# Performance work log

Measured on AMD Instinct MI355X. Metric: run time of the kernel, lower is better.

The kernel has to match this reference:

```python
import jax, jax.numpy as jnp
import numpy as np
import math

B, S, D = 2, 2048, 1024
H, DK, DV = 16, 64, 64  # head_count, query_size, value_size; H*DV == D
NEG_INF = -jnp.inf


def setup_inputs() -> dict:
    key = jax.random.key(0)
    ks = jax.random.split(key, 10)
    sc = 0.02
    return {
        "input": jax.random.normal(ks[0], (B, S, D), dtype=jnp.float32),
        "padding_mask": jnp.zeros((B, S), dtype=jnp.float32),  # 0 = valid, 1 = padded
        "wq_w": jax.random.normal(ks[1], (H * DK, D), dtype=jnp.float32) * sc,
        "wq_b": jnp.zeros((H * DK,), dtype=jnp.float32),
        "wk_w": jax.random.normal(ks[2], (H * DK, D), dtype=jnp.float32) * sc,
        "wk_b": jnp.zeros((H * DK,), dtype=jnp.float32),
        "wv_w": jax.random.normal(ks[3], (H * DV, D), dtype=jnp.float32) * sc,
        "wv_b": jnp.zeros((H * DV,), dtype=jnp.float32),
        "fin_w": jax.random.normal(ks[4], (D, H * DV), dtype=jnp.float32) * sc,
        "fin_b": jnp.zeros((D,), dtype=jnp.float32),
    }


def reference(input, padding_mask, wq_w, wq_b, wk_w, wk_b, wv_w, wv_b, fin_w, fin_b):
    b, s, _ = input.shape
    # projections -> [b, h, s, d]
    Q = (input @ wq_w.T + wq_b).reshape(b, s, H, DK).transpose(0, 2, 1, 3)
    K = (input @ wk_w.T + wk_b).reshape(b, s, H, DK).transpose(0, 2, 1, 3)
    V = (input @ wv_w.T + wv_b).reshape(b, s, H, DV).transpose(0, 2, 1, 3)

    # padding mask: pad*(-inf), nan_to_num(0*inf -> 0); broadcast over query dim
    pad = jnp.where(padding_mask > 0, NEG_INF, 0.0)[:, None, None, :]  # [b,1,1,s]
    i = jnp.arange(s)
    causal = jnp.where(i[None, :] < i[:, None] + 1, 0.0, NEG_INF)  # [s,s]
    mask = pad + causal[None, None, :, :]

    # (QK^T + mask) / sqrt(dk), softmax over keys
    logits = (jnp.einsum("bhqd,bhkd->bhqk", Q, K) + mask) / math.sqrt(DK)
    attn = jax.nn.softmax(logits, axis=-1)
    out = jnp.einsum("bhqk,bhkd->bqhd", attn, V).reshape(b, s, H * DV)
    return out @ fin_w.T + fin_b
```

## Files before the change

kernel.cpp:

```cpp
#include <hip/hip_runtime.h>


typedef __bf16 bf16;
typedef __bf16 bf16x8 __attribute__((ext_vector_type(8)));
typedef __bf16 bf16x4 __attribute__((ext_vector_type(4)));
typedef float  f32x4  __attribute__((ext_vector_type(4)));

#define B_  2
#define S_  2048
#define D_  1024
#define H_  16
#define HD  64
#define NEG_BIG (-3.0e38f)
#define SCALE_LOG2E 0.1803368801111204f

__device__ __forceinline__ void lds16(const void* g, void* l) {
    __builtin_amdgcn_global_load_lds((const __attribute__((address_space(1))) void*)g,
                                     (__attribute__((address_space(3))) void*)l, 16, 0, 0);
}

__device__ __forceinline__ f32x4 mfma16(bf16x8 a, bf16x8 b, f32x4 c) {
    return __builtin_amdgcn_mfma_f32_16x16x32_bf16(a, b, c, 0, 0, 0);
}

__global__ __launch_bounds__(256) void convert_k(const float* __restrict__ X,
                                                 const float* __restrict__ wq,
                                                 const float* __restrict__ wk,
                                                 const float* __restrict__ wv,
                                                 const float* __restrict__ wo,
                                                 bf16* __restrict__ dst) {
    const int gid = blockIdx.x * 256 + threadIdx.x;
    const int i   = gid * 4;
    const float* src;
    int off;
    if      (i < (4 << 20)) { src = X;  off = 0; }
    else if (i < (5 << 20)) { src = wq; off = 4 << 20; }
    else if (i < (6 << 20)) { src = wk; off = 5 << 20; }
    else if (i < (7 << 20)) { src = wv; off = 6 << 20; }
    else                    { src = wo; off = 7 << 20; }
    const float4 v = *(const float4*)(src + (i - off));
    bf16x4 p;
    p[0] = (bf16)v.x; p[1] = (bf16)v.y; p[2] = (bf16)v.z; p[3] = (bf16)v.w;
    *(bf16x4*)(dst + i) = p;
}

__global__ __launch_bounds__(256) void gemm_qkv(const bf16* __restrict__ A,
                                                const bf16* __restrict__ Wq,
                                                const bf16* __restrict__ Wk,
                                                const bf16* __restrict__ Wv,
                                                const float* __restrict__ bq,
                                                const float* __restrict__ bk,
                                                const float* __restrict__ bv,
                                                bf16* __restrict__ Qw,
                                                bf16* __restrict__ Kw,
                                                bf16* __restrict__ Vw) {
    constexpr int K = 1024;
    __shared__ bf16 sA[128 * 32];
    __shared__ bf16 sB[128 * 32];
    const int tid  = threadIdx.x;
    const int l15  = tid & 15;
    const int quad = (tid & 63) >> 4;
    const int wid  = tid >> 6;
    const int seg  = blockIdx.x >> 3;
    const int bn   = blockIdx.x & 7;
    const int bm   = blockIdx.y;
    const int wm   = (wid >> 1) * 64;
    const int wn   = (wid & 1) * 64;

    const bf16* W    = (seg == 0) ? Wq : (seg == 1) ? Wk : Wv;
    const float* bias = (seg == 0) ? bq : (seg == 1) ? bk : bv;

    const bf16* Ab = A + (size_t)bm * 128 * K;
    const bf16* Wb = W + (size_t)bn * 128 * K;

    f32x4 acc[4][4] = {};

    for (int k0 = 0; k0 < K; k0 += 32) {
        __syncthreads();
        #pragma unroll
        for (int it = 0; it < 2; ++it) {
            int c = it * 256 + tid;
            int row = c >> 2, c8 = c & 3;
            lds16(Ab + row * K + k0 + c8 * 8, (char*)sA + c * 16);
            lds16(Wb + row * K + k0 + c8 * 8, (char*)sB + c * 16);
        }
        __syncthreads();
        bf16x8 af[4], bfr[4];
        #pragma unroll
        for (int i = 0; i < 4; ++i)
            af[i] = *(const bf16x8*)&sA[(wm + i * 16 + l15) * 32 + quad * 8];
        #pragma unroll
        for (int i = 0; i < 4; ++i)
            bfr[i] = *(const bf16x8*)&sB[(wn + i * 16 + l15) * 32 + quad * 8];
        #pragma unroll
        for (int mi = 0; mi < 4; ++mi)
            #pragma unroll
            for (int ni = 0; ni < 4; ++ni)
                acc[mi][ni] = mfma16(af[mi], bfr[ni], acc[mi][ni]);
    }

    #pragma unroll
    for (int ni = 0; ni < 4; ++ni) {
        const int n  = bn * 128 + wn + ni * 16 + l15;
        const float bv_ = bias[n];
        const int h = n >> 6;
        #pragma unroll
        for (int mi = 0; mi < 4; ++mi) {
            const int m0 = bm * 128 + wm + mi * 16 + quad * 4;
            if (seg == 2) {
                const int dv = n & 63;
                const int b = m0 >> 11, s = m0 & 2047;
                bf16x4 pack;
                #pragma unroll
                for (int r = 0; r < 4; ++r) pack[r] = (bf16)(acc[mi][ni][r] + bv_);
                *(bf16x4*)&Vw[(((size_t)(b * H_ + h) * HD + dv) << 11) + s] = pack;
            } else {
                bf16* C = (seg == 0) ? Qw : Kw;
                const int dk = n & 63;
                #pragma unroll
                for (int r = 0; r < 4; ++r) {
                    const int m = m0 + r, b = m >> 11, s = m & 2047;
                    C[(((size_t)(b * H_ + h) << 11) + s) * HD + dk] =
                        (bf16)(acc[mi][ni][r] + bv_);
                }
            }
        }
    }
}

__global__ __launch_bounds__(256) void gemm_fin(const bf16* __restrict__ A,
                                                const bf16* __restrict__ W,
                                                const float* __restrict__ bias,
                                                float* __restrict__ C) {
    constexpr int N = 1024, K = 1024;
    __shared__ bf16 sA[128 * 32];
    __shared__ bf16 sB[128 * 32];
    const int tid  = threadIdx.x;
    const int l15  = tid & 15;
    const int quad = (tid & 63) >> 4;
    const int wid  = tid >> 6;
    const int bm   = blockIdx.x >> 3;
    const int bn   = blockIdx.x & 7;
    const int wm   = (wid >> 1) * 64;
    const int wn   = (wid & 1) * 64;

    const bf16* Ab = A + (size_t)bm * 128 * K;
    const bf16* Wb = W + (size_t)bn * 128 * K;

    f32x4 acc[4][4] = {};

    for (int k0 = 0; k0 < K; k0 += 32) {
        __syncthreads();
        #pragma unroll
        for (int it = 0; it < 2; ++it) {
            int c = it * 256 + tid;
            int row = c >> 2, c8 = c & 3;
            lds16(Ab + row * K + k0 + c8 * 8, (char*)sA + c * 16);
            lds16(Wb + row * K + k0 + c8 * 8, (char*)sB + c * 16);
        }
        __syncthreads();
        bf16x8 af[4], bfr[4];
        #pragma unroll
        for (int i = 0; i < 4; ++i)
            af[i] = *(const bf16x8*)&sA[(wm + i * 16 + l15) * 32 + quad * 8];
        #pragma unroll
        for (int i = 0; i < 4; ++i)
            bfr[i] = *(const bf16x8*)&sB[(wn + i * 16 + l15) * 32 + quad * 8];
        #pragma unroll
        for (int mi = 0; mi < 4; ++mi)
            #pragma unroll
            for (int ni = 0; ni < 4; ++ni)
                acc[mi][ni] = mfma16(af[mi], bfr[ni], acc[mi][ni]);
    }

    #pragma unroll
    for (int ni = 0; ni < 4; ++ni) {
        const int n  = bn * 128 + wn + ni * 16 + l15;
        const float bv = bias[n];
        #pragma unroll
        for (int mi = 0; mi < 4; ++mi) {
            const int m0 = bm * 128 + wm + mi * 16 + quad * 4;
            #pragma unroll
            for (int r = 0; r < 4; ++r)
                C[(size_t)(m0 + r) * N + n] = acc[mi][ni][r] + bv;
        }
    }
}

__global__ __launch_bounds__(512, 4) void attn_k(const bf16* __restrict__ Q,
                                                 const bf16* __restrict__ K,
                                                 const bf16* __restrict__ Vt,
                                                 const float* __restrict__ pmask,
                                                 bf16* __restrict__ Aout) {
    __shared__ bf16 sK_[2 * 128 * 32];
    __shared__ bf16 sV[4 * 64 * 32];
    __shared__ bf16 sPQ[4 * 128 * 32];
    const int tid  = threadIdx.x;
    const int l15  = tid & 15;
    const int quad = (tid & 63) >> 4;
    const int wid  = tid >> 6;
    const int idx  = blockIdx.x >> 5;
    const int qt   = (idx < 8) ? (15 - idx) : (idx - 8);
    const int bh   = blockIdx.x & 31;
    const int b    = bh >> 4;
    const int h    = bh & 15;

    const bf16* Qg = Q + ((size_t)bh * S_ + qt * 128) * HD;
    #pragma unroll
    for (int it = 0; it < 2; ++it) {
        int c = it * 512 + tid;
        int pl = c >> 9, row = (c >> 2) & 127, c8 = c & 3;
        lds16(Qg + row * HD + pl * 32 + c8 * 8, (char*)sPQ + c * 16);
    }
    __syncthreads();
    bf16x8 aq[2];
    #pragma unroll
    for (int kk = 0; kk < 2; ++kk)
        aq[kk] = *(const bf16x8*)&sPQ[(kk * 128 + wid * 16 + l15) * 32 + quad * 8];

    float m_i[4], l_i[4];
    f32x4 o[4] = {};
    #pragma unroll
    for (int r = 0; r < 4; ++r) { m_i[r] = NEG_BIG; l_i[r] = 0.f; }

    for (int kt = 0; kt <= qt; ++kt) {
        __syncthreads();
        const bf16* Kg = K  + ((size_t)bh * S_ + kt * 128) * HD;
        const bf16* Vg = Vt + (size_t)bh * HD * S_ + kt * 128;
        #pragma unroll
        for (int it = 0; it < 2; ++it) {
            int c = it * 512 + tid;
            { int pl = c >> 9, row = (c >> 2) & 127, c8 = c & 3;
              lds16(Kg + row * HD + pl * 32 + c8 * 8, (char*)sK_ + c * 16); }
            { int kc = c >> 8, dv = (c >> 2) & 63, c8 = c & 3;
              lds16(Vg + dv * S_ + kc * 32 + c8 * 8, (char*)sV + c * 16); }
        }
        __syncthreads();

        f32x4 s[8] = {};
        #pragma unroll
        for (int tc = 0; tc < 8; ++tc) {
            #pragma unroll
            for (int kk = 0; kk < 2; ++kk) {
                bf16x8 bk = *(const bf16x8*)
                    &sK_[(kk * 128 + tc * 16 + l15) * 32 + quad * 8];
                s[tc] = mfma16(aq[kk], bk, s[tc]);
            }
        }

        float pmadd[8];
        #pragma unroll
        for (int tc = 0; tc < 8; ++tc) {
            int kg = kt * 128 + tc * 16 + l15;
            pmadd[tc] = (pmask[b * S_ + kg] > 0.f) ? NEG_BIG : 0.f;
        }
        const bool diag = (kt == qt);
        #pragma unroll
        for (int tc = 0; tc < 8; ++tc)
            #pragma unroll
            for (int r = 0; r < 4; ++r) {
                float v = s[tc][r] * SCALE_LOG2E + pmadd[tc];
                if (diag) {
                    int kl = tc * 16 + l15;
                    int ql = wid * 16 + quad * 4 + r;
                    if (kl > ql) v = NEG_BIG;
                }
                s[tc][r] = v;
            }

        #pragma unroll
        for (int r = 0; r < 4; ++r) {
            float rm = s[0][r];
            #pragma unroll
            for (int tc = 1; tc < 8; ++tc) rm = fmaxf(rm, s[tc][r]);
            rm = fmaxf(rm, __shfl_xor(rm, 1, 16));
            rm = fmaxf(rm, __shfl_xor(rm, 2, 16));
            rm = fmaxf(rm, __shfl_xor(rm, 4, 16));
            rm = fmaxf(rm, __shfl_xor(rm, 8, 16));
            float mn    = fmaxf(m_i[r], rm);
            float alpha = exp2f(m_i[r] - mn);
            m_i[r]      = mn;
            float rs = 0.f;
            #pragma unroll
            for (int tc = 0; tc < 8; ++tc) {
                float p = exp2f(s[tc][r] - mn);
                s[tc][r] = p;
                rs += p;
            }
            rs += __shfl_xor(rs, 1, 16);
            rs += __shfl_xor(rs, 2, 16);
            rs += __shfl_xor(rs, 4, 16);
            rs += __shfl_xor(rs, 8, 16);
            l_i[r] = l_i[r] * alpha + rs;
            #pragma unroll
            for (int vc = 0; vc < 4; ++vc) o[vc][r] *= alpha;
        }

        #pragma unroll
        for (int tc = 0; tc < 8; ++tc)
            #pragma unroll
            for (int r = 0; r < 4; ++r) {
                int ql = wid * 16 + quad * 4 + r;
                int kl = tc * 16 + l15;
                sPQ[((kl >> 5) * 128 + ql) * 32 + (kl & 31)] = (bf16)s[tc][r];
            }
        __syncthreads();

        #pragma unroll
        for (int kc = 0; kc < 4; ++kc) {
            bf16x8 ap = *(const bf16x8*)
                &sPQ[(kc * 128 + wid * 16 + l15) * 32 + quad * 8];
            #pragma unroll
            for (int vc = 0; vc < 4; ++vc) {
                bf16x8 bv = *(const bf16x8*)
                    &sV[(kc * 64 + vc * 16 + l15) * 32 + quad * 8];
                o[vc] = mfma16(ap, bv, o[vc]);
            }
        }
    }

    #pragma unroll
    for (int r = 0; r < 4; ++r) {
        float inv = 1.f / l_i[r];
        int q = qt * 128 + wid * 16 + quad * 4 + r;
        size_t base = ((size_t)b * S_ + q) * D_ + h * HD;
        #pragma unroll
        for (int vc = 0; vc < 4; ++vc)
            Aout[base + vc * 16 + l15] = (bf16)(o[vc][r] * inv);
    }
}

extern "C" void kernel_launch(void* const* d_in, const int* in_sizes, int n_in,
                              void* d_out, int out_size, void* d_ws, size_t ws_size,
                              hipStream_t stream) {
    const float* X   = (const float*)d_in[0];
    const float* pm  = (const float*)d_in[1];
    const float* wq  = (const float*)d_in[2];
    const float* bq  = (const float*)d_in[3];
    const float* wk  = (const float*)d_in[4];
    const float* bk  = (const float*)d_in[5];
    const float* wv  = (const float*)d_in[6];
    const float* bvb = (const float*)d_in[7];
    const float* wo  = (const float*)d_in[8];
    const float* bo  = (const float*)d_in[9];
    float* out = (float*)d_out;

    char* ws = (char*)d_ws;
    bf16* Xb  = (bf16*)(ws);
    bf16* Wqb = (bf16*)(ws + (8u  << 20));
    bf16* Wkb = (bf16*)(ws + (10u << 20));
    bf16* Wvb = (bf16*)(ws + (12u << 20));
    bf16* Wob = (bf16*)(ws + (14u << 20));
    bf16* Qw  = (bf16*)(ws + (16u << 20));
    bf16* Kw  = (bf16*)(ws + (24u << 20));
    bf16* Vw  = (bf16*)(ws + (32u << 20));
    bf16* Aw  = (bf16*)(ws + (40u << 20));

    convert_k<<<dim3(8192), dim3(256), 0, stream>>>(X, wq, wk, wv, wo, Xb);
    gemm_qkv<<<dim3(24, 32), dim3(256), 0, stream>>>(Xb, Wqb, Wkb, Wvb,
                                                     bq, bk, bvb, Qw, Kw, Vw);
    attn_k<<<dim3(512), dim3(512), 0, stream>>>(Qw, Kw, Vw, pm, Aw);
    gemm_fin<<<dim3(256), dim3(256), 0, stream>>>(Aw, Wob, bo, out);
}
```

Before: 221.8 us.

## Prefetch next K/V tile into registers and transpose S for row-local softmax

The attention kernel now loads the next K/V tile from global memory into registers while the current tile is being computed, then stores those registers into LDS at the start of the next iteration, replacing the synchronous LDS-direct loads. The QK^T MFMA operands are swapped so each lane holds one query row's scores. This lets the row max and row sum use two cross-quad shuffles instead of four per row, and lets P be written as packed bf16x4 into a padded row-major LDS buffer. The padding mask is read as a float4. The cost is more registers for the prefetch buffers and extra shuffles to broadcast alpha and 1/l into the output layout, which may reduce occupancy.

```diff
diff --git a/kernel.cpp b/kernel.cpp
--- a/kernel.cpp
+++ b/kernel.cpp
@@ -187,6 +187,7 @@
     }
 }
 
+#define PSTRIDE 136
 __global__ __launch_bounds__(512, 4) void attn_k(const bf16* __restrict__ Q,
                                                  const bf16* __restrict__ K,
                                                  const bf16* __restrict__ Vt,
@@ -194,7 +195,7 @@
                                                  bf16* __restrict__ Aout) {
     __shared__ bf16 sK_[2 * 128 * 32];
     __shared__ bf16 sV[4 * 64 * 32];
-    __shared__ bf16 sPQ[4 * 128 * 32];
+    __shared__ bf16 sP[128 * PSTRIDE];
     const int tid  = threadIdx.x;
     const int l15  = tid & 15;
     const int quad = (tid & 63) >> 4;
@@ -210,30 +211,50 @@
     for (int it = 0; it < 2; ++it) {
         int c = it * 512 + tid;
         int pl = c >> 9, row = (c >> 2) & 127, c8 = c & 3;
-        lds16(Qg + row * HD + pl * 32 + c8 * 8, (char*)sPQ + c * 16);
+        lds16(Qg + row * HD + pl * 32 + c8 * 8, (char*)sP + c * 16);
+    }
+    bf16x8 kreg[2], vreg[2];
+    {
+        const bf16* Kg = K  + (size_t)bh * S_ * HD;
+        const bf16* Vg = Vt + (size_t)bh * HD * S_;
+        #pragma unroll
+        for (int it = 0; it < 2; ++it) {
+            int c = it * 512 + tid;
+            int pl = c >> 9, row = (c >> 2) & 127, c8 = c & 3;
+            kreg[it] = *(const bf16x8*)(Kg + row * HD + pl * 32 + c8 * 8);
+            int kc = c >> 8, dv = (c >> 2) & 63;
+            vreg[it] = *(const bf16x8*)(Vg + dv * S_ + kc * 32 + c8 * 8);
+        }
     }
     __syncthreads();
     bf16x8 aq[2];
     #pragma unroll
     for (int kk = 0; kk < 2; ++kk)
-        aq[kk] = *(const bf16x8*)&sPQ[(kk * 128 + wid * 16 + l15) * 32 + quad * 8];
-
-    float m_i[4], l_i[4];
+        aq[kk] = *(const bf16x8*)&sP[(kk * 128 + wid * 16 + l15) * 32 + quad * 8];
+
+    float m_i = NEG_BIG, l_i = 0.f;
     f32x4 o[4] = {};
-    #pragma unroll
-    for (int r = 0; r < 4; ++r) { m_i[r] = NEG_BIG; l_i[r] = 0.f; }
+    const int qg = wid * 16 + l15;
 
     for (int kt = 0; kt <= qt; ++kt) {
         __syncthreads();
-        const bf16* Kg = K  + ((size_t)bh * S_ + kt * 128) * HD;
-        const bf16* Vg = Vt + (size_t)bh * HD * S_ + kt * 128;
         #pragma unroll
         for (int it = 0; it < 2; ++it) {
             int c = it * 512 + tid;
-            { int pl = c >> 9, row = (c >> 2) & 127, c8 = c & 3;
-              lds16(Kg + row * HD + pl * 32 + c8 * 8, (char*)sK_ + c * 16); }
-            { int kc = c >> 8, dv = (c >> 2) & 63, c8 = c & 3;
-              lds16(Vg + dv * S_ + kc * 32 + c8 * 8, (char*)sV + c * 16); }
+            *(bf16x8*)((char*)sK_ + c * 16) = kreg[it];
+            *(bf16x8*)((char*)sV  + c * 16) = vreg[it];
+        }
+        if (kt < qt) {
+            const bf16* Kg = K  + ((size_t)bh * S_ + (kt + 1) * 128) * HD;
+            const bf16* Vg = Vt + (size_t)bh * HD * S_ + (kt + 1) * 128;
+            #pragma unroll
+            for (int it = 0; it < 2; ++it) {
+                int c = it * 512 + tid;
+                int pl = c >> 9, row = (c >> 2) & 127, c8 = c & 3;
+                kreg[it] = *(const bf16x8*)(Kg + row * HD + pl * 32 + c8 * 8);
+                int kc = c >> 8, dv = (c >> 2) & 63;
+                vreg[it] = *(const bf16x8*)(Vg + dv * S_ + kc * 32 + c8 * 8);
+            }
         }
         __syncthreads();
 
@@ -242,74 +263,69 @@
         for (int tc = 0; tc < 8; ++tc) {
             #pragma unroll
             for (int kk = 0; kk < 2; ++kk) {
-                bf16x8 bk = *(const bf16x8*)
+                bf16x8 kb = *(const bf16x8*)
                     &sK_[(kk * 128 + tc * 16 + l15) * 32 + quad * 8];
-                s[tc] = mfma16(aq[kk], bk, s[tc]);
-            }
-        }
-
-        float pmadd[8];
+                s[tc] = mfma16(kb, aq[kk], s[tc]);
+            }
+        }
+
+        const bool diag = (kt == qt);
         #pragma unroll
         for (int tc = 0; tc < 8; ++tc) {
-            int kg = kt * 128 + tc * 16 + l15;
-            pmadd[tc] = (pmask[b * S_ + kg] > 0.f) ? NEG_BIG : 0.f;
-        }
-        const bool diag = (kt == qt);
+            const float4 pv = *(const float4*)
+                &pmask[b * S_ + kt * 128 + tc * 16 + quad * 4];
+            #pragma unroll
+            for (int r = 0; r < 4; ++r) {
+                float v = s[tc][r] * SCALE_LOG2E;
+                if (((const float*)&pv)[r] > 0.f) v = NEG_BIG;
+                if (diag && (tc * 16 + quad * 4 + r > qg)) v = NEG_BIG;
+                s[tc][r] = v;
+            }
+        }
+
+        float rm = s[0][0];
         #pragma unroll
         for (int tc = 0; tc < 8; ++tc)
             #pragma unroll
+            for (int r = 0; r < 4; ++r) rm = fmaxf(rm, s[tc][r]);
+        rm = fmaxf(rm, __shfl_xor(rm, 16));
+        rm = fmaxf(rm, __shfl_xor(rm, 32));
+        const float mn    = fmaxf(m_i, rm);
+        const float alpha = exp2f(m_i - mn);
+        m_i = mn;
+        float rs = 0.f;
+        #pragma unroll
+        for (int tc = 0; tc < 8; ++tc)
+            #pragma unroll
             for (int r = 0; r < 4; ++r) {
-                float v = s[tc][r] * SCALE_LOG2E + pmadd[tc];
-                if (diag) {
-                    int kl = tc * 16 + l15;
-                    int ql = wid * 16 + quad * 4 + r;
-                    if (kl > ql) v = NEG_BIG;
-                }
-                s[tc][r] = v;
-            }
-
-        #pragma unroll
-        for (int r = 0; r < 4; ++r) {
-            float rm = s[0][r];
-            #pragma unroll
-            for (int tc = 1; tc < 8; ++tc) rm = fmaxf(rm, s[tc][r]);
-            rm = fmaxf(rm, __shfl_xor(rm, 1, 16));
-            rm = fmaxf(rm, __shfl_xor(rm, 2, 16));
-            rm = fmaxf(rm, __shfl_xor(rm, 4, 16));
-            rm = fmaxf(rm, __shfl_xor(rm, 8, 16));
-            float mn    = fmaxf(m_i[r], rm);
-            float alpha = exp2f(m_i[r] - mn);
-            m_i[r]      = mn;
-            float rs = 0.f;
-            #pragma unroll
-            for (int tc = 0; tc < 8; ++tc) {
                 float p = exp2f(s[tc][r] - mn);
                 s[tc][r] = p;
                 rs += p;
             }
-            rs += __shfl_xor(rs, 1, 16);
-            rs += __shfl_xor(rs, 2, 16);
-            rs += __shfl_xor(rs, 4, 16);
-            rs += __shfl_xor(rs, 8, 16);
-            l_i[r] = l_i[r] * alpha + rs;
-            #pragma unroll
-            for (int vc = 0; vc < 4; ++vc) o[vc][r] *= alpha;
-        }
-
-        #pragma unroll
-        for (int tc = 0; tc < 8; ++tc)
-            #pragma unroll
-            for (int r = 0; r < 4; ++r) {
-                int ql = wid * 16 + quad * 4 + r;
-                int kl = tc * 16 + l15;
-                sPQ[((kl >> 5) * 128 + ql) * 32 + (kl & 31)] = (bf16)s[tc][r];
-            }
+        rs += __shfl_xor(rs, 16);
+        rs += __shfl_xor(rs, 32);
+        l_i = l_i * alpha + rs;
+
+        #pragma unroll
+        for (int tc = 0; tc < 8; ++tc) {
+            bf16x4 pk;
+            #pragma unroll
+            for (int r = 0; r < 4; ++r) pk[r] = (bf16)s[tc][r];
+            *(bf16x4*)&sP[qg * PSTRIDE + tc * 16 + quad * 4] = pk;
+        }
+
+        #pragma unroll
+        for (int r = 0; r < 4; ++r) {
+            float ar = __shfl(alpha, quad * 4 + r, 16);
+            #pragma unroll
+            for (int vc = 0; vc < 4; ++vc) o[vc][r] *= ar;
+        }
         __syncthreads();
 
         #pragma unroll
         for (int kc = 0; kc < 4; ++kc) {
             bf16x8 ap = *(const bf16x8*)
-                &sPQ[(kc * 128 + wid * 16 + l15) * 32 + quad * 8];
+                &sP[(wid * 16 + l15) * PSTRIDE + kc * 32 + quad * 8];
             #pragma unroll
             for (int vc = 0; vc < 4; ++vc) {
                 bf16x8 bv = *(const bf16x8*)
@@ -319,14 +335,15 @@
         }
     }
 
+    const float inv = 1.f / l_i;
     #pragma unroll
     for (int r = 0; r < 4; ++r) {
-        float inv = 1.f / l_i[r];
+        float ir = __shfl(inv, quad * 4 + r, 16);
         int q = qt * 128 + wid * 16 + quad * 4 + r;
         size_t base = ((size_t)b * S_ + q) * D_ + h * HD;
         #pragma unroll
         for (int vc = 0; vc < 4; ++vc)
-            Aout[base + vc * 16 + l15] = (bf16)(o[vc][r] * inv);
+            Aout[base + vc * 16 + l15] = (bf16)(o[vc][r] * ir);
     }
 }
 
```

After: 224.3 us. About the same (+1.1%).

## Halve attention query tile, register-prefetch K/V, and split output GEMM tiles

Applied to the files above, without the earlier changes.

The attention kernel now uses 64-query tiles with 256 threads and 1024 blocks, using a new four-way tile ordering for load balance. It prefetches the next K/V tile into registers while the current tile is computed, and writes P to LDS in two halves with a new layout. The final GEMM switches to 64x128 tiles so it launches twice as many blocks for better CU occupancy. The costs are more redundant K/V loads per query row and higher register pressure from the prefetch buffers.

```diff
diff --git a/kernel.cpp b/kernel.cpp
--- a/kernel.cpp
+++ b/kernel.cpp
@@ -2,8 +2,8 @@
 
 
 typedef __bf16 bf16;
+typedef __bf16 bf16x4 __attribute__((ext_vector_type(4)));
 typedef __bf16 bf16x8 __attribute__((ext_vector_type(8)));
-typedef __bf16 bf16x4 __attribute__((ext_vector_type(4)));
 typedef float  f32x4  __attribute__((ext_vector_type(4)));
 
 #define B_  2
@@ -133,7 +133,7 @@
                                                 const float* __restrict__ bias,
                                                 float* __restrict__ C) {
     constexpr int N = 1024, K = 1024;
-    __shared__ bf16 sA[128 * 32];
+    __shared__ bf16 sA[64 * 32];
     __shared__ bf16 sB[128 * 32];
     const int tid  = threadIdx.x;
     const int l15  = tid & 15;
@@ -141,33 +141,36 @@
     const int wid  = tid >> 6;
     const int bm   = blockIdx.x >> 3;
     const int bn   = blockIdx.x & 7;
-    const int wm   = (wid >> 1) * 64;
-    const int wn   = (wid & 1) * 64;
-
-    const bf16* Ab = A + (size_t)bm * 128 * K;
+    const int wm   = (wid & 1) * 32;
+    const int wn   = (wid >> 1) * 64;
+
+    const bf16* Ab = A + (size_t)bm * 64 * K;
     const bf16* Wb = W + (size_t)bn * 128 * K;
 
-    f32x4 acc[4][4] = {};
+    f32x4 acc[2][4] = {};
 
     for (int k0 = 0; k0 < K; k0 += 32) {
         __syncthreads();
+        {
+            int c = tid, row = c >> 2, c8 = c & 3;
+            lds16(Ab + row * K + k0 + c8 * 8, (char*)sA + c * 16);
+        }
         #pragma unroll
         for (int it = 0; it < 2; ++it) {
             int c = it * 256 + tid;
             int row = c >> 2, c8 = c & 3;
-            lds16(Ab + row * K + k0 + c8 * 8, (char*)sA + c * 16);
             lds16(Wb + row * K + k0 + c8 * 8, (char*)sB + c * 16);
         }
         __syncthreads();
-        bf16x8 af[4], bfr[4];
-        #pragma unroll
-        for (int i = 0; i < 4; ++i)
+        bf16x8 af[2], bfr[4];
+        #pragma unroll
+        for (int i = 0; i < 2; ++i)
             af[i] = *(const bf16x8*)&sA[(wm + i * 16 + l15) * 32 + quad * 8];
         #pragma unroll
         for (int i = 0; i < 4; ++i)
             bfr[i] = *(const bf16x8*)&sB[(wn + i * 16 + l15) * 32 + quad * 8];
         #pragma unroll
-        for (int mi = 0; mi < 4; ++mi)
+        for (int mi = 0; mi < 2; ++mi)
             #pragma unroll
             for (int ni = 0; ni < 4; ++ni)
                 acc[mi][ni] = mfma16(af[mi], bfr[ni], acc[mi][ni]);
@@ -178,8 +181,8 @@
         const int n  = bn * 128 + wn + ni * 16 + l15;
         const float bv = bias[n];
         #pragma unroll
-        for (int mi = 0; mi < 4; ++mi) {
-            const int m0 = bm * 128 + wm + mi * 16 + quad * 4;
+        for (int mi = 0; mi < 2; ++mi) {
+            const int m0 = bm * 64 + wm + mi * 16 + quad * 4;
             #pragma unroll
             for (int r = 0; r < 4; ++r)
                 C[(size_t)(m0 + r) * N + n] = acc[mi][ni][r] + bv;
@@ -187,66 +190,89 @@
     }
 }
 
-__global__ __launch_bounds__(512, 4) void attn_k(const bf16* __restrict__ Q,
+__global__ __launch_bounds__(256, 4) void attn_k(const bf16* __restrict__ Q,
                                                  const bf16* __restrict__ K,
                                                  const bf16* __restrict__ Vt,
                                                  const float* __restrict__ pmask,
                                                  bf16* __restrict__ Aout) {
     __shared__ bf16 sK_[2 * 128 * 32];
     __shared__ bf16 sV[4 * 64 * 32];
-    __shared__ bf16 sPQ[4 * 128 * 32];
+    __shared__ bf16 sP[4096];
     const int tid  = threadIdx.x;
     const int l15  = tid & 15;
     const int quad = (tid & 63) >> 4;
     const int wid  = tid >> 6;
-    const int idx  = blockIdx.x >> 5;
-    const int qt   = (idx < 8) ? (15 - idx) : (idx - 8);
+    const int j    = blockIdx.x >> 5;
     const int bh   = blockIdx.x & 31;
     const int b    = bh >> 4;
     const int h    = bh & 15;
-
-    const bf16* Qg = Q + ((size_t)bh * S_ + qt * 128) * HD;
+    const int a_  = j >> 3, bq_ = j & 7;
+    const int qt  = (a_ == 0) ? (31 - bq_) : (a_ == 1) ? bq_
+                  : (a_ == 2) ? (23 - bq_) : (8 + bq_);
+    const int nkt = (qt >> 1) + 1;
+
+    const bf16* Qg = Q + ((size_t)bh * S_ + qt * 64) * HD;
     #pragma unroll
     for (int it = 0; it < 2; ++it) {
-        int c = it * 512 + tid;
+        int c = it * 256 + tid;
+        int pl = c >> 8, row = (c >> 2) & 63, c8 = c & 3;
+        lds16(Qg + row * HD + pl * 32 + c8 * 8, (char*)sK_ + c * 16);
+    }
+    const bf16* Kg = K  + (size_t)bh * S_ * HD;
+    const bf16* Vg = Vt + (size_t)bh * HD * S_;
+    bf16x8 kreg[4], vreg[4];
+    #pragma unroll
+    for (int it = 0; it < 4; ++it) {
+        int c = it * 256 + tid;
         int pl = c >> 9, row = (c >> 2) & 127, c8 = c & 3;
-        lds16(Qg + row * HD + pl * 32 + c8 * 8, (char*)sPQ + c * 16);
+        kreg[it] = *(const bf16x8*)(Kg + row * HD + pl * 32 + c8 * 8);
+        int kc = c >> 8, dv = (c >> 2) & 63;
+        vreg[it] = *(const bf16x8*)(Vg + dv * S_ + kc * 32 + c8 * 8);
     }
     __syncthreads();
     bf16x8 aq[2];
     #pragma unroll
     for (int kk = 0; kk < 2; ++kk)
-        aq[kk] = *(const bf16x8*)&sPQ[(kk * 128 + wid * 16 + l15) * 32 + quad * 8];
+        aq[kk] = *(const bf16x8*)&sK_[(kk * 64 + wid * 16 + l15) * 32 + quad * 8];
 
     float m_i[4], l_i[4];
     f32x4 o[4] = {};
     #pragma unroll
     for (int r = 0; r < 4; ++r) { m_i[r] = NEG_BIG; l_i[r] = 0.f; }
-
-    for (int kt = 0; kt <= qt; ++kt) {
-        __syncthreads();
-        const bf16* Kg = K  + ((size_t)bh * S_ + kt * 128) * HD;
-        const bf16* Vg = Vt + (size_t)bh * HD * S_ + kt * 128;
-        #pragma unroll
-        for (int it = 0; it < 2; ++it) {
-            int c = it * 512 + tid;
-            { int pl = c >> 9, row = (c >> 2) & 127, c8 = c & 3;
-              lds16(Kg + row * HD + pl * 32 + c8 * 8, (char*)sK_ + c * 16); }
-            { int kc = c >> 8, dv = (c >> 2) & 63, c8 = c & 3;
-              lds16(Vg + dv * S_ + kc * 32 + c8 * 8, (char*)sV + c * 16); }
+    const int qrow = wid * 16 + quad * 4;
+    const int qg0  = qt * 64 + qrow;
+
+    for (int kt = 0; kt < nkt; ++kt) {
+        __syncthreads();
+        #pragma unroll
+        for (int it = 0; it < 4; ++it) {
+            int c = it * 256 + tid;
+            *(bf16x8*)((char*)sK_ + c * 16) = kreg[it];
+            *(bf16x8*)((char*)sV  + c * 16) = vreg[it];
+        }
+        if (kt + 1 < nkt) {
+            const bf16* Kg2 = Kg + (size_t)(kt + 1) * 128 * HD;
+            const bf16* Vg2 = Vg + (kt + 1) * 128;
+            #pragma unroll
+            for (int it = 0; it < 4; ++it) {
+                int c = it * 256 + tid;
+                int pl = c >> 9, row = (c >> 2) & 127, c8 = c & 3;
+                kreg[it] = *(const bf16x8*)(Kg2 + row * HD + pl * 32 + c8 * 8);
+                int kc = c >> 8, dv = (c >> 2) & 63;
+                vreg[it] = *(const bf16x8*)(Vg2 + dv * S_ + kc * 32 + c8 * 8);
+            }
         }
         __syncthreads();
 
         f32x4 s[8] = {};
         #pragma unroll
-        for (int tc = 0; tc < 8; ++tc) {
+        for (int tc = 0; tc < 8; ++tc)
             #pragma unroll
             for (int kk = 0; kk < 2; ++kk) {
                 bf16x8 bk = *(const bf16x8*)
                     &sK_[(kk * 128 + tc * 16 + l15) * 32 + quad * 8];
                 s[tc] = mfma16(aq[kk], bk, s[tc]);
             }
-        }
 
         float pmadd[8];
         #pragma unroll
@@ -254,17 +280,13 @@
             int kg = kt * 128 + tc * 16 + l15;
             pmadd[tc] = (pmask[b * S_ + kg] > 0.f) ? NEG_BIG : 0.f;
         }
-        const bool diag = (kt == qt);
+        const bool lastt = (kt == nkt - 1);
         #pragma unroll
         for (int tc = 0; tc < 8; ++tc)
             #pragma unroll
             for (int r = 0; r < 4; ++r) {
                 float v = s[tc][r] * SCALE_LOG2E + pmadd[tc];
-                if (diag) {
-                    int kl = tc * 16 + l15;
-                    int ql = wid * 16 + quad * 4 + r;
-                    if (kl > ql) v = NEG_BIG;
-                }
+                if (lastt && (kt * 128 + tc * 16 + l15 > qg0 + r)) v = NEG_BIG;
                 s[tc][r] = v;
             }
 
@@ -297,24 +319,27 @@
         }
 
         #pragma unroll
-        for (int tc = 0; tc < 8; ++tc)
-            #pragma unroll
-            for (int r = 0; r < 4; ++r) {
-                int ql = wid * 16 + quad * 4 + r;
-                int kl = tc * 16 + l15;
-                sPQ[((kl >> 5) * 128 + ql) * 32 + (kl & 31)] = (bf16)s[tc][r];
-            }
-        __syncthreads();
-
-        #pragma unroll
-        for (int kc = 0; kc < 4; ++kc) {
-            bf16x8 ap = *(const bf16x8*)
-                &sPQ[(kc * 128 + wid * 16 + l15) * 32 + quad * 8];
-            #pragma unroll
-            for (int vc = 0; vc < 4; ++vc) {
-                bf16x8 bv = *(const bf16x8*)
-                    &sV[(kc * 64 + vc * 16 + l15) * 32 + quad * 8];
-                o[vc] = mfma16(ap, bv, o[vc]);
+        for (int hf = 0; hf < 2; ++hf) {
+            #pragma unroll
+            for (int tc4 = 0; tc4 < 4; ++tc4) {
+                const int tc = hf * 4 + tc4;
+                const int keyh = tc4 * 16 + l15;
+                const int base = (keyh >> 3) * 512 + (keyh & 7);
+                #pragma unroll
+                for (int r = 0; r < 4; ++r)
+                    sP[base + (qrow + r) * 8] = (bf16)s[tc][r];
+            }
+            #pragma unroll
+            for (int c2 = 0; c2 < 2; ++c2) {
+                bf16x8 ap = *(const bf16x8*)
+                    &sP[(c2 * 4 + quad) * 512 + (wid * 16 + l15) * 8];
+                const int kc = hf * 2 + c2;
+                #pragma unroll
+                for (int vc = 0; vc < 4; ++vc) {
+                    bf16x8 bv = *(const bf16x8*)
+                        &sV[(kc * 64 + vc * 16 + l15) * 32 + quad * 8];
+                    o[vc] = mfma16(ap, bv, o[vc]);
+                }
             }
         }
     }
@@ -322,8 +347,7 @@
     #pragma unroll
     for (int r = 0; r < 4; ++r) {
         float inv = 1.f / l_i[r];
-        int q = qt * 128 + wid * 16 + quad * 4 + r;
-        size_t base = ((size_t)b * S_ + q) * D_ + h * HD;
+        size_t base = ((size_t)b * S_ + qg0 + r) * D_ + h * HD;
         #pragma unroll
         for (int vc = 0; vc < 4; ++vc)
             Aout[base + vc * 16 + l15] = (bf16)(o[vc][r] * inv);
@@ -359,6 +383,6 @@
     convert_k<<<dim3(8192), dim3(256), 0, stream>>>(X, wq, wk, wv, wo, Xb);
     gemm_qkv<<<dim3(24, 32), dim3(256), 0, stream>>>(Xb, Wqb, Wkb, Wvb,
                                                      bq, bk, bvb, Qw, Kw, Vw);
-    attn_k<<<dim3(512), dim3(512), 0, stream>>>(Qw, Kw, Vw, pm, Aw);
-    gemm_fin<<<dim3(256), dim3(256), 0, stream>>>(Aw, Wob, bo, out);
-}
+    attn_k<<<dim3(1024), dim3(256), 0, stream>>>(Qw, Kw, Vw, pm, Aw);
+    gemm_fin<<<dim3(512), dim3(256), 0, stream>>>(Aw, Wob, bo, out);
+}
```

Measured after the change: 268.4 us. 21.0% more time.
